# Kernel tuning notes

Measured on AMD Instinct MI355X. Metric: run time of the kernel, lower is better.

Reference implementation:

```python
import jax, jax.numpy as jnp
import numpy as np

N, C, T, V = 64, 64, 256, 25
R, O = C // 8, 64  # rel_channels, out_channels
ALPHA = 1.0


def setup_inputs() -> dict:
    key = jax.random.key(0)
    ks = jax.random.split(key, 10)
    s = 0.05
    return {
        "x": jax.random.normal(ks[0], (N, C, T, V), dtype=jnp.float32),
        "A": jax.random.normal(ks[1], (V, V), dtype=jnp.float32),
        "w1": jax.random.normal(ks[2], (R, C), dtype=jnp.float32) * s,
        "b1": jnp.zeros((R,), dtype=jnp.float32),
        "w2": jax.random.normal(ks[3], (R, C), dtype=jnp.float32) * s,
        "b2": jnp.zeros((R,), dtype=jnp.float32),
        "w3": jax.random.normal(ks[4], (O, C), dtype=jnp.float32) * s,
        "b3": jnp.zeros((O,), dtype=jnp.float32),
        "w4": jax.random.normal(ks[5], (O, R), dtype=jnp.float32) * s,
        "b4": jnp.zeros((O,), dtype=jnp.float32),
    }


def reference(x, A, w1, b1, w2, b2, w3, b3, w4, b4):
    # x: (N, C, T, V)
    # conv1/conv2 are 1x1 convs followed by mean over T -> (N, R, V)
    x1 = jnp.einsum('nctv,rc->nrv', x, w1) / x.shape[2] + b1[:, None]
    x2 = jnp.einsum('nctv,rc->nrv', x, w2) / x.shape[2] + b2[:, None]
    # conv3: 1x1 conv -> (N, O, T, V)
    x3 = jnp.einsum('nctv,oc->notv', x, w3) + b3[:, None, None]
    # outer-difference attention over joints: (N, R, V, V)
    att = jnp.tanh(x1[:, :, :, None] - x2[:, :, None, :])
    # conv4 channel mix (R->O), scale, add adjacency: (N, O, V, V)
    m = jnp.einsum('nruv,or->nouv', att, w4) + b4[:, None, None]
    m = m * ALPHA + A[None, None, :, :]
    # aggregation: einsum('ncuv,nctv->nctu')
    out = jnp.einsum('ncuv,nctv->nctu', m, x3)
    return out
```

## Files before the change

kernel.cpp:

```cpp
#include <hip/hip_runtime.h>

#define NN 64
#define CC 64
#define TT 256
#define VV 25
#define RR 8
#define OO 64
#define PLANE 6400
#define SX 226

__global__ __launch_bounds__(256) void k_xsum(const float* __restrict__ x,
                                              float* __restrict__ xsum,
                                              const float* __restrict__ w3,
                                              float* __restrict__ w3t) {
  int nc = blockIdx.x;
  int tid = threadIdx.x;
  if (blockIdx.x < 16) {
    int k = blockIdx.x * 256 + tid;
    int c = k >> 6, o = k & 63;
    w3t[k] = w3[o * 64 + c];
  }
  const float* src = x + (size_t)nc * PLANE;
  __shared__ float s[PLANE];
#pragma unroll
  for (int k = 0; k < 25; ++k) s[k * 256 + tid] = src[k * 256 + tid];
  __syncthreads();
  if (tid < VV) {
    float a0 = 0.f, a1 = 0.f, a2 = 0.f, a3 = 0.f;
    for (int t = 0; t < TT; t += 4) {
      a0 += s[(t + 0) * VV + tid];
      a1 += s[(t + 1) * VV + tid];
      a2 += s[(t + 2) * VV + tid];
      a3 += s[(t + 3) * VV + tid];
    }
    xsum[nc * VV + tid] = (a0 + a1) + (a2 + a3);
  }
}

__global__ __launch_bounds__(256) void k_build_m(
    const float* __restrict__ xsum, const float* __restrict__ A,
    const float* __restrict__ w1, const float* __restrict__ b1,
    const float* __restrict__ w2, const float* __restrict__ b2,
    const float* __restrict__ w4, const float* __restrict__ b4,
    float* __restrict__ mp) {
  int n = blockIdx.x;
  int og = blockIdx.y;
  __shared__ float xs[CC * VV];
  __shared__ float sx1[RR * VV];
  __shared__ float sx2[RR * VV];
  __shared__ float att[RR * 625];
  int tid = threadIdx.x;
  const float* xsn = xsum + n * (CC * VV);
  for (int k = tid; k < CC * VV; k += 256) xs[k] = xsn[k];
  __syncthreads();
  if (tid < RR * VV) {
    int r = tid / VV, v = tid % VV;
    float a1 = 0.f, a2 = 0.f;
#pragma unroll
    for (int c = 0; c < CC; ++c) {
      float xv = xs[c * VV + v];
      a1 = fmaf(w1[r * CC + c], xv, a1);
      a2 = fmaf(w2[r * CC + c], xv, a2);
    }
    sx1[tid] = a1 * (1.f / 256.f) + b1[r];
    sx2[tid] = a2 * (1.f / 256.f) + b2[r];
  }
  __syncthreads();
  for (int k = tid; k < RR * 625; k += 256) {
    int r = k / 625, uv = k % 625;
    int u = uv / VV, v = uv % VV;
    att[k] = tanhf(sx1[r * VV + u] - sx2[r * VV + v]);
  }
  __syncthreads();
  for (int k = tid; k < 16 * 625; k += 256) {
    int o = og * 16 + k / 625, vu = k % 625;
    int v = vu / VV, u = vu % VV;
    float a = b4[o] + A[u * VV + v];
#pragma unroll
    for (int r = 0; r < RR; ++r)
      a = fmaf(w4[o * RR + r], att[r * 625 + u * VV + v], a);
    mp[(((size_t)n * OO + o) * VV + v) * 32 + u] = a;
  }
}

__global__ __launch_bounds__(256, 2) void k_fused(
    const float* __restrict__ x, const float* __restrict__ w3t,
    const float* __restrict__ b3, const float* __restrict__ mp,
    float* __restrict__ out) {
  int n = blockIdx.y;
  int t0 = blockIdx.x * 8;
  __shared__ float s[OO * SX];
  int tid = threadIdx.x;

  if (tid < 200) {
    const float* xp = x + (size_t)n * CC * PLANE + t0 * VV + tid;
    float acc[OO];
#pragma unroll
    for (int o = 0; o < OO; ++o) acc[o] = b3[o];
#pragma unroll 2
    for (int c = 0; c < CC; ++c) {
      float xv = xp[(size_t)c * PLANE];
      const float* w = w3t + c * OO;
#pragma unroll
      for (int o = 0; o < OO; ++o) acc[o] = fmaf(w[o], xv, acc[o]);
    }
#pragma unroll
    for (int o = 0; o < OO; ++o) s[o * SX + tid] = acc[o];
  }
  __syncthreads();

  {
    int o = tid >> 2, tq = tid & 3;
    const float* xA = s + o * SX + tq * VV;
    const float* xB = xA + 4 * VV;
    const float* mb = mp + (size_t)(n * OO + o) * VV * 32;
    float accA[VV], accB[VV];
#pragma unroll
    for (int u = 0; u < VV; ++u) {
      accA[u] = 0.f;
      accB[u] = 0.f;
    }
#pragma unroll 2
    for (int v = 0; v < VV; ++v) {
      float xa = xA[v];
      float xb = xB[v];
      const float* mr = mb + v * 32;
#pragma unroll
      for (int u = 0; u < VV; ++u) {
        float mv = mr[u];
        accA[u] = fmaf(mv, xa, accA[u]);
        accB[u] = fmaf(mv, xb, accB[u]);
      }
    }
    __syncthreads();
#pragma unroll
    for (int u = 0; u < VV; ++u) {
      s[o * SX + tq * VV + u] = accA[u];
      s[o * SX + (tq + 4) * VV + u] = accB[u];
    }
  }
  __syncthreads();

  float* ob = out + (size_t)n * OO * PLANE + t0 * VV;
  for (int k = tid; k < OO * 200; k += 256) {
    int oo = k / 200, p = k - oo * 200;
    ob[(size_t)oo * PLANE + p] = s[oo * SX + p];
  }
}

extern "C" void kernel_launch(void* const* d_in, const int* in_sizes, int n_in,
                              void* d_out, int out_size, void* d_ws,
                              size_t ws_size, hipStream_t stream) {
  const float* x = (const float*)d_in[0];
  const float* A = (const float*)d_in[1];
  const float* w1 = (const float*)d_in[2];
  const float* b1 = (const float*)d_in[3];
  const float* w2 = (const float*)d_in[4];
  const float* b2 = (const float*)d_in[5];
  const float* w3 = (const float*)d_in[6];
  const float* b3 = (const float*)d_in[7];
  const float* w4 = (const float*)d_in[8];
  const float* b4 = (const float*)d_in[9];
  float* out = (float*)d_out;
  float* ws = (float*)d_ws;

  float* xsum = ws;
  float* w3t = ws + 102400;
  float* mp = ws + 106496;

  k_xsum<<<NN * CC, 256, 0, stream>>>(x, xsum, w3, w3t);
  k_build_m<<<dim3(NN, 4), 256, 0, stream>>>(xsum, A, w1, b1, w2, b2, w4, b4,
                                             mp);
  k_fused<<<dim3(TT / 8, NN), 256, 0, stream>>>(x, w3t, b3, mp, out);
}
```

Baseline: 323.4 us.

## Retile aggregation stage by u-quarters with float4 m loads, parallelize T-sum

The aggregation stage now gives each thread 8 time steps by 8 output joints (u split into quarters padded to 32), loading m with float4 and x3 values from shared memory. Before, each thread handled 2 time steps across all 25 u. The reduction over T in k_xsum is spread over 200 threads with a second-level sum instead of 25 threads looping serially. The conv3 loop batches 8 channel loads ahead of the FMAs, and occupancy is raised to 3 blocks per CU with a tighter shared stride. The risks are wasted lanes from padding u to 32 and register pressure under the stricter launch bound.

```diff
diff --git a/kernel.cpp b/kernel.cpp
--- a/kernel.cpp
+++ b/kernel.cpp
@@ -7,7 +7,7 @@
 #define RR 8
 #define OO 64
 #define PLANE 6400
-#define SX 226
+#define SX 201
 
 __global__ __launch_bounds__(256) void k_xsum(const float* __restrict__ x,
                                               float* __restrict__ xsum,
@@ -21,19 +21,27 @@
     w3t[k] = w3[o * 64 + c];
   }
   const float* src = x + (size_t)nc * PLANE;
-  __shared__ float s[PLANE];
+  __shared__ float s[PLANE + 256];
 #pragma unroll
   for (int k = 0; k < 25; ++k) s[k * 256 + tid] = src[k * 256 + tid];
   __syncthreads();
+  if (tid < 200) {
+    int tg = tid / 25, v = tid - tg * 25;
+    float a0 = 0.f, a1 = 0.f, a2 = 0.f, a3 = 0.f;
+    for (int k = 0; k < 32; k += 4) {
+      a0 += s[(tg + 8 * (k + 0)) * VV + v];
+      a1 += s[(tg + 8 * (k + 1)) * VV + v];
+      a2 += s[(tg + 8 * (k + 2)) * VV + v];
+      a3 += s[(tg + 8 * (k + 3)) * VV + v];
+    }
+    s[PLANE + tid] = (a0 + a1) + (a2 + a3);
+  }
+  __syncthreads();
   if (tid < VV) {
-    float a0 = 0.f, a1 = 0.f, a2 = 0.f, a3 = 0.f;
-    for (int t = 0; t < TT; t += 4) {
-      a0 += s[(t + 0) * VV + tid];
-      a1 += s[(t + 1) * VV + tid];
-      a2 += s[(t + 2) * VV + tid];
-      a3 += s[(t + 3) * VV + tid];
-    }
-    xsum[nc * VV + tid] = (a0 + a1) + (a2 + a3);
+    float a = 0.f;
+#pragma unroll
+    for (int g = 0; g < 8; ++g) a += s[PLANE + g * VV + tid];
+    xsum[nc * VV + tid] = a;
   }
 }
 
@@ -83,7 +91,7 @@
   }
 }
 
-__global__ __launch_bounds__(256, 2) void k_fused(
+__global__ __launch_bounds__(256, 3) void k_fused(
     const float* __restrict__ x, const float* __restrict__ w3t,
     const float* __restrict__ b3, const float* __restrict__ mp,
     float* __restrict__ out) {
@@ -97,12 +105,16 @@
     float acc[OO];
 #pragma unroll
     for (int o = 0; o < OO; ++o) acc[o] = b3[o];
-#pragma unroll 2
-    for (int c = 0; c < CC; ++c) {
-      float xv = xp[(size_t)c * PLANE];
-      const float* w = w3t + c * OO;
+    for (int c = 0; c < CC; c += 8) {
+      float xv[8];
 #pragma unroll
-      for (int o = 0; o < OO; ++o) acc[o] = fmaf(w[o], xv, acc[o]);
+      for (int j = 0; j < 8; ++j) xv[j] = xp[(size_t)(c + j) * PLANE];
+#pragma unroll
+      for (int j = 0; j < 8; ++j) {
+        const float* w = w3t + (c + j) * OO;
+#pragma unroll
+        for (int o = 0; o < OO; ++o) acc[o] = fmaf(w[o], xv[j], acc[o]);
+      }
     }
 #pragma unroll
     for (int o = 0; o < OO; ++o) s[o * SX + tid] = acc[o];
@@ -110,34 +122,41 @@
   __syncthreads();
 
   {
-    int o = tid >> 2, tq = tid & 3;
-    const float* xA = s + o * SX + tq * VV;
-    const float* xB = xA + 4 * VV;
-    const float* mb = mp + (size_t)(n * OO + o) * VV * 32;
-    float accA[VV], accB[VV];
+    int o = tid >> 2, uq = tid & 3;
+    const float* mb = mp + (size_t)(n * OO + o) * (VV * 32) + uq * 8;
+    const float* xb = s + o * SX;
+    float acc[8][8];
 #pragma unroll
-    for (int u = 0; u < VV; ++u) {
-      accA[u] = 0.f;
-      accB[u] = 0.f;
-    }
+    for (int t = 0; t < 8; ++t)
+#pragma unroll
+      for (int j = 0; j < 8; ++j) acc[t][j] = 0.f;
 #pragma unroll 2
     for (int v = 0; v < VV; ++v) {
-      float xa = xA[v];
-      float xb = xB[v];
-      const float* mr = mb + v * 32;
+      float4 m0 = *(const float4*)(mb + v * 32);
+      float4 m1 = *(const float4*)(mb + v * 32 + 4);
+      float xt[8];
 #pragma unroll
-      for (int u = 0; u < VV; ++u) {
-        float mv = mr[u];
-        accA[u] = fmaf(mv, xa, accA[u]);
-        accB[u] = fmaf(mv, xb, accB[u]);
+      for (int t = 0; t < 8; ++t) xt[t] = xb[t * VV + v];
+#pragma unroll
+      for (int t = 0; t < 8; ++t) {
+        acc[t][0] = fmaf(m0.x, xt[t], acc[t][0]);
+        acc[t][1] = fmaf(m0.y, xt[t], acc[t][1]);
+        acc[t][2] = fmaf(m0.z, xt[t], acc[t][2]);
+        acc[t][3] = fmaf(m0.w, xt[t], acc[t][3]);
+        acc[t][4] = fmaf(m1.x, xt[t], acc[t][4]);
+        acc[t][5] = fmaf(m1.y, xt[t], acc[t][5]);
+        acc[t][6] = fmaf(m1.z, xt[t], acc[t][6]);
+        acc[t][7] = fmaf(m1.w, xt[t], acc[t][7]);
       }
     }
     __syncthreads();
 #pragma unroll
-    for (int u = 0; u < VV; ++u) {
-      s[o * SX + tq * VV + u] = accA[u];
-      s[o * SX + (tq + 4) * VV + u] = accB[u];
-    }
+    for (int t = 0; t < 8; ++t)
+#pragma unroll
+      for (int j = 0; j < 8; ++j) {
+        int u = uq * 8 + j;
+        if (u < VV) s[o * SX + t * VV + u] = acc[t][j];
+      }
   }
   __syncthreads();
 
```

Measured after the change: 317.3 us. No clear change (-1.9%).
